# Kernel tuning notes

Hardware: AMD Instinct MI355X
Metric: run time of the kernel (lower is better)

The kernel has to match this reference:

```python
import jax, jax.numpy as jnp
import numpy as np

D_MODEL = 1024
N_HEADS = 16
HEAD_DIM = D_MODEL // N_HEADS
B, T = 4, 2048


def setup_inputs() -> dict:
    key = jax.random.key(0)
    ks = jax.random.split(key, 5)
    x = jax.random.normal(ks[0], (B, T, D_MODEL), dtype=jnp.float32)
    # causal mask; masked_fill(mask == 0, -inf) => attend where mask is True
    mask = jnp.tril(jnp.ones((T, T), dtype=bool))
    # parameters (torch Linear: y = x @ W.T + b); store already-transposed [in, out]
    s_in = 1.0 / np.sqrt(D_MODEL)
    Wqkv = jax.random.uniform(ks[1], (D_MODEL, 3 * D_MODEL), jnp.float32, -s_in, s_in)
    bqkv = jax.random.uniform(ks[2], (3 * D_MODEL,), jnp.float32, -s_in, s_in)
    Wout = jax.random.uniform(ks[3], (D_MODEL, D_MODEL), jnp.float32, -s_in, s_in)
    bout = jax.random.uniform(ks[4], (D_MODEL,), jnp.float32, -s_in, s_in)
    return {"x": x, "mask": mask, "Wqkv": Wqkv, "bqkv": bqkv, "Wout": Wout, "bout": bout}


def reference(x, mask, Wqkv, bqkv, Wout, bout):
    Bq, Tq, C = x.shape
    qkv = x @ Wqkv + bqkv                       # [B, T, 3C]
    q, k, v = jnp.split(qkv, 3, axis=-1)
    def split_heads(t):
        return t.reshape(Bq, Tq, N_HEADS, HEAD_DIM).transpose(0, 2, 1, 3)  # [B,H,T,d]
    q, k, v = split_heads(q), split_heads(k), split_heads(v)
    scale = 1.0 / np.sqrt(HEAD_DIM).astype(np.float32)
    att = jnp.einsum("bhqd,bhkd->bhqk", q, k) * scale  # [B,H,T,T]
    att = jnp.where(mask, att, -jnp.inf)
    att = jax.nn.softmax(att, axis=-1)
    out = jnp.einsum("bhqk,bhkd->bhqd", att, v)         # [B,H,T,d]
    out = out.transpose(0, 2, 1, 3).reshape(Bq, Tq, C)  # [B,T,C]
    return out @ Wout + bout
```

## Files before the change

kernel.cpp:

```cpp
#include <hip/hip_runtime.h>
#include <hip/hip_bf16.h>
#include <cstdint>
#include <cstddef>

#define DMODEL 1024
#define NHEADS 16
#define HDIM 64
#define BATCH 4
#define SEQ 2048
#define MROWS (BATCH*SEQ)
#define N3 (3*DMODEL)
#define BHCNT (BATCH*NHEADS)

typedef __attribute__((ext_vector_type(8))) short short8;
typedef __attribute__((ext_vector_type(4))) short short4v;
typedef __attribute__((ext_vector_type(4))) float f32x4;
typedef __attribute__((ext_vector_type(4))) unsigned int uint4v;

static __device__ __forceinline__ short f2bf(float f) {
  unsigned int u = __builtin_bit_cast(unsigned int, f);
  return (short)((u + 0x7fffu + ((u >> 16) & 1u)) >> 16);
}

static __device__ __forceinline__ unsigned int pack_bf16(float lo, float hi) {
  unsigned int r;
  asm("v_cvt_pk_bf16_f32 %0, %1, %2" : "=v"(r) : "v"(lo), "v"(hi));
  return r;
}

static __device__ __forceinline__ void permlane32_swap(unsigned int& a, unsigned int& b) {
  asm("v_permlane32_swap_b32 %0, %1" : "+v"(a), "+v"(b));
}
static __device__ __forceinline__ void permlane16_swap(unsigned int& a, unsigned int& b) {
  asm("v_permlane16_swap_b32 %0, %1" : "+v"(a), "+v"(b));
}

static __device__ __forceinline__ float fast_exp2(float x) {
#if __has_builtin(__builtin_amdgcn_exp2f)
  return __builtin_amdgcn_exp2f(x);
#else
  return exp2f(x);
#endif
}

static __device__ __forceinline__ void gload16(const void* g, void* l) {
  __builtin_amdgcn_global_load_lds(
      (const __attribute__((address_space(1))) unsigned int*)g,
      (__attribute__((address_space(3))) unsigned int*)l, 16, 0, 0);
}

__global__ __launch_bounds__(256) void cast_x_kernel(
    const float* __restrict__ in, short* __restrict__ out, int n) {
  int i = (blockIdx.x * 256 + threadIdx.x) * 4;
  if (i + 3 < n) {
    float4 v = *(const float4*)(in + i);
    short4v s;
    s[0] = f2bf(v.x); s[1] = f2bf(v.y); s[2] = f2bf(v.z); s[3] = f2bf(v.w);
    *(short4v*)(out + i) = s;
  }
}

__global__ __launch_bounds__(256) void transpose_cast_kernel(
    const float* __restrict__ in, short* __restrict__ out, int K, int N) {
  __shared__ float tile[32][33];
  int n0 = blockIdx.x * 32, k0 = blockIdx.y * 32;
  int tx = threadIdx.x, ty = threadIdx.y;
#pragma unroll
  for (int i = 0; i < 4; ++i)
    tile[ty + i * 8][tx] = in[(size_t)(k0 + ty + i * 8) * N + (n0 + tx)];
  __syncthreads();
#pragma unroll
  for (int i = 0; i < 4; ++i)
    out[(size_t)(n0 + ty + i * 8) * K + (k0 + tx)] = f2bf(tile[tx][ty + i * 8]);
}

template <int EPI>
__global__ __launch_bounds__(256, 2) void gemm128_kernel(
    const short* __restrict__ A, const short* __restrict__ Bt,
    const float* __restrict__ bias, float* __restrict__ foutp,
    short* __restrict__ q_out, short* __restrict__ k_out,
    short* __restrict__ v_out, int Mdim, int Ndim, int Kdim) {
  __shared__ __align__(16) short As[128 * 32];
  __shared__ __align__(16) short Bs[128 * 32];
  const int tid = threadIdx.x;
  const int lane = tid & 63;
  const int w = tid >> 6;
  const int wr = w >> 1, wc = w & 1;
  const int nwg = gridDim.x * gridDim.y;
  const int lin = blockIdx.y * gridDim.x + blockIdx.x;
  const int tile = (lin & 7) * (nwg >> 3) + (lin >> 3);
  const int row0 = (tile / gridDim.x) * 128;
  const int col0 = (tile % gridDim.x) * 128;
  const int lrow = lane & 15, lkg = lane >> 4;

  f32x4 acc[4][4];
#pragma unroll
  for (int i = 0; i < 4; ++i)
#pragma unroll
    for (int j = 0; j < 4; ++j) acc[i][j] = (f32x4){0.f, 0.f, 0.f, 0.f};

  const short* Ab = A + (size_t)row0 * Kdim;
  const short* Bb = Bt + (size_t)col0 * Kdim;
  const int sr = tid >> 2;
  const int sc = (tid & 3) * 8;

  for (int kt = 0; kt < Kdim; kt += 32) {
    gload16(Ab + (size_t)sr * Kdim + kt + sc, As + tid * 8);
    gload16(Ab + (size_t)(sr + 64) * Kdim + kt + sc, As + 2048 + tid * 8);
    gload16(Bb + (size_t)sr * Kdim + kt + sc, Bs + tid * 8);
    gload16(Bb + (size_t)(sr + 64) * Kdim + kt + sc, Bs + 2048 + tid * 8);
    __syncthreads();
    short8 af[4], bfr[4];
#pragma unroll
    for (int i = 0; i < 4; ++i)
      af[i] = *(const short8*)(As + (wr * 64 + i * 16 + lrow) * 32 + lkg * 8);
#pragma unroll
    for (int j = 0; j < 4; ++j)
      bfr[j] = *(const short8*)(Bs + (wc * 64 + j * 16 + lrow) * 32 + lkg * 8);
#pragma unroll
    for (int i = 0; i < 4; ++i)
#pragma unroll
      for (int j = 0; j < 4; ++j)
        acc[i][j] = __builtin_amdgcn_mfma_f32_16x16x32_bf16(af[i], bfr[j], acc[i][j], 0, 0, 0);
    __syncthreads();
  }

#pragma unroll
  for (int i = 0; i < 4; ++i) {
#pragma unroll
    for (int j = 0; j < 4; ++j) {
      const int gn = col0 + wc * 64 + j * 16 + lrow;
      const int gmb = row0 + wr * 64 + i * 16 + lkg * 4;
      float vr[4];
#pragma unroll
      for (int r = 0; r < 4; ++r) vr[r] = acc[i][j][r] + bias[gn];
      if (EPI == 0) {
        const int which = gn >> 10;
        const int hh = (gn >> 6) & 15;
        const int dd = gn & 63;
        const int b = gmb >> 11;
        const int tt0 = gmb & 2047;
        const size_t bh = (size_t)b * NHEADS + hh;
        if (which == 0) {
#pragma unroll
          for (int r = 0; r < 4; ++r)
            q_out[(bh * SEQ + tt0 + r) * HDIM + dd] = f2bf(vr[r] * 0.125f);
        } else if (which == 1) {
#pragma unroll
          for (int r = 0; r < 4; ++r)
            k_out[(bh * SEQ + tt0 + r) * HDIM + (dd ^ (((tt0 + r) & 7) << 3))] = f2bf(vr[r]);
        } else {
          short4v pk;
#pragma unroll
          for (int r = 0; r < 4; ++r) pk[r] = f2bf(vr[r]);
          *(short4v*)(v_out + (bh * HDIM + dd) * SEQ + (tt0 ^ ((dd & 7) << 3))) = pk;
        }
      } else {
#pragma unroll
        for (int r = 0; r < 4; ++r)
          foutp[(size_t)(gmb + r) * Ndim + gn] = vr[r];
      }
    }
  }
}

__global__ __launch_bounds__(256, 4) void attn_kernel(
    const short* __restrict__ qb, const short* __restrict__ kb,
    const short* __restrict__ vb, short* __restrict__ aout) {
  __shared__ __align__(16) short Ks2[2][64 * 64];
  __shared__ __align__(16) short Vs2[2][64 * 64];
  const int tid = threadIdx.x;
  const int lane = tid & 63;
  const int w = tid >> 6;
  const int lin = blockIdx.y * gridDim.x + blockIdx.x;
  const int tile = ((lin & 7) << 7) + (lin >> 3);
  const int bh = tile >> 4;
  const int ip = tile & 15;
  const int heavy_q0 = (31 - ip) * 64;
  const int light_q0 = ip * 64;
  const int qw0 = (w < 2) ? heavy_q0 + w * 32 : light_q0 + (w - 2) * 32;
  const int lrow = lane & 15, lkg = lane >> 4;

  const short* kbase = kb + (size_t)bh * SEQ * HDIM;
  const short* vbase = vb + (size_t)bh * HDIM * SEQ;

  short8 qf[2][2];
#pragma unroll
  for (int rb = 0; rb < 2; ++rb) {
    const short* qrow = qb + ((size_t)bh * SEQ + qw0 + rb * 16 + lrow) * HDIM;
    qf[rb][0] = *(const short8*)(qrow + lkg * 8);
    qf[rb][1] = *(const short8*)(qrow + 32 + lkg * 8);
  }

  f32x4 o[2][4];
  float mr[2], lsum[2];
#pragma unroll
  for (int rb = 0; rb < 2; ++rb) {
#pragma unroll
    for (int g = 0; g < 4; ++g) o[rb][g] = (f32x4){0.f, 0.f, 0.f, 0.f};
    mr[rb] = -__builtin_inff();
    lsum[rb] = 0.f;
  }

  const int ntile = 32 - ip;

  {
    short* Kd = Ks2[0]; short* Vd = Vs2[0];
#pragma unroll
    for (int i = 0; i < 2; ++i)
      gload16(kbase + i * 2048 + tid * 8, Kd + i * 2048 + tid * 8);
#pragma unroll
    for (int i = 0; i < 2; ++i)
      gload16(vbase + (size_t)(32 * i + (tid >> 3)) * SEQ + (tid & 7) * 8,
              Vd + i * 2048 + tid * 8);
  }
  __syncthreads();

  int cur = 0;
  for (int it = 0; it < ntile; ++it) {
    const int kt = it * 64;
    if (it + 1 < ntile) {
      const int k2 = kt + 64;
      short* Kd = Ks2[cur ^ 1]; short* Vd = Vs2[cur ^ 1];
#pragma unroll
      for (int i = 0; i < 2; ++i)
        gload16(kbase + (size_t)k2 * HDIM + i * 2048 + tid * 8, Kd + i * 2048 + tid * 8);
#pragma unroll
      for (int i = 0; i < 2; ++i)
        gload16(vbase + (size_t)(32 * i + (tid >> 3)) * SEQ + k2 + (tid & 7) * 8,
                Vd + i * 2048 + tid * 8);
    }
    if (kt <= qw0 + 31) {
      const short* Ks = Ks2[cur];
      const short* Vs = Vs2[cur];
      f32x4 s[2][4];
#pragma unroll
      for (int rb = 0; rb < 2; ++rb)
#pragma unroll
        for (int f = 0; f < 4; ++f) s[rb][f] = (f32x4){0.f, 0.f, 0.f, 0.f};

      __builtin_amdgcn_s_setprio(1);
#pragma unroll
      for (int c = 0; c < 2; ++c) {
#pragma unroll
        for (int f = 0; f < 4; ++f) {
          const int krow = f * 16 + lrow;
          const int kel = (c * 32 + lkg * 8) ^ ((krow & 7) << 3);
          short8 kf = *(const short8*)(Ks + krow * 64 + kel);
          s[0][f] = __builtin_amdgcn_mfma_f32_16x16x32_bf16(kf, qf[0][c], s[0][f], 0, 0, 0);
          s[1][f] = __builtin_amdgcn_mfma_f32_16x16x32_bf16(kf, qf[1][c], s[1][f], 0, 0, 0);
        }
      }
      __builtin_amdgcn_s_setprio(0);

      if (kt + 63 > qw0) {
#pragma unroll
        for (int rb = 0; rb < 2; ++rb) {
          const int qq = qw0 + rb * 16 + lrow;
#pragma unroll
          for (int f = 0; f < 4; ++f) {
            const int kg = kt + f * 16 + lkg * 4;
#pragma unroll
            for (int r = 0; r < 4; ++r)
              if (kg + r > qq) s[rb][f][r] = -__builtin_inff();
          }
        }
      }

      const float L2E = 1.44269504088896340736f;
      float pm[2];
#pragma unroll
      for (int rb = 0; rb < 2; ++rb) {
        float p = fmaxf(fmaxf(fmaxf(s[rb][0][0], s[rb][0][1]), fmaxf(s[rb][0][2], s[rb][0][3])),
                        fmaxf(fmaxf(s[rb][1][0], s[rb][1][1]), fmaxf(s[rb][1][2], s[rb][1][3])));
        p = fmaxf(p, fmaxf(fmaxf(fmaxf(s[rb][2][0], s[rb][2][1]), fmaxf(s[rb][2][2], s[rb][2][3])),
                           fmaxf(fmaxf(s[rb][3][0], s[rb][3][1]), fmaxf(s[rb][3][2], s[rb][3][3]))));
        p = fmaxf(p, __shfl_xor(p, 16));
        p = fmaxf(p, __shfl_xor(p, 32));
        pm[rb] = p;
      }
      const float mn0 = fmaxf(mr[0], pm[0]);
      const float mn1 = fmaxf(mr[1], pm[1]);
      if (!__all(pm[0] <= mr[0] && pm[1] <= mr[1])) {
        const float a0 = fast_exp2((mr[0] - mn0) * L2E);
        const float a1 = fast_exp2((mr[1] - mn1) * L2E);
        lsum[0] *= a0;
        lsum[1] *= a1;
#pragma unroll
        for (int r = 0; r < 4; ++r) {
          const float s0 = __shfl(a0, lkg * 4 + r, 16);
          const float s1 = __shfl(a1, lkg * 4 + r, 16);
#pragma unroll
          for (int g = 0; g < 4; ++g) { o[0][g][r] *= s0; o[1][g][r] *= s1; }
        }
      }
      mr[0] = mn0; mr[1] = mn1;

      unsigned int q32[2][4][2];
#pragma unroll
      for (int rb = 0; rb < 2; ++rb) {
        const float mn = rb ? mn1 : mn0;
        float rs = 0.f;
#pragma unroll
        for (int f = 0; f < 4; ++f)
#pragma unroll
          for (int r = 0; r < 4; ++r) {
            const float p = fast_exp2((s[rb][f][r] - mn) * L2E);
            s[rb][f][r] = p;
            rs += p;
          }
        rs += __shfl_xor(rs, 16);
        rs += __shfl_xor(rs, 32);
        lsum[rb] += rs;
#pragma unroll
        for (int f = 0; f < 4; ++f) {
          q32[rb][f][0] = pack_bf16(s[rb][f][0], s[rb][f][1]);
          q32[rb][f][1] = pack_bf16(s[rb][f][2], s[rb][f][3]);
        }
      }

      __builtin_amdgcn_s_setprio(1);
#pragma unroll
      for (int c = 0; c < 2; ++c) {
        uint4v pw0, pw1;
#pragma unroll
        for (int h = 0; h < 2; ++h) {
          unsigned int a0 = q32[0][2 * c][h], b0 = q32[0][2 * c + 1][h];
          permlane32_swap(a0, b0);
          permlane16_swap(a0, b0);
          pw0[h] = a0; pw0[2 + h] = b0;
          unsigned int a1 = q32[1][2 * c][h], b1 = q32[1][2 * c + 1][h];
          permlane32_swap(a1, b1);
          permlane16_swap(a1, b1);
          pw1[h] = a1; pw1[2 + h] = b1;
        }
        const short8 pf0 = __builtin_bit_cast(short8, pw0);
        const short8 pf1 = __builtin_bit_cast(short8, pw1);
#pragma unroll
        for (int g = 0; g < 4; ++g) {
          const int vrow = g * 16 + lrow;
          const int vel = (c * 32 + lkg * 8) ^ ((vrow & 7) << 3);
          short8 vf = *(const short8*)(Vs + vrow * 64 + vel);
          o[0][g] = __builtin_amdgcn_mfma_f32_16x16x32_bf16(pf0, vf, o[0][g], 0, 0, 0);
          o[1][g] = __builtin_amdgcn_mfma_f32_16x16x32_bf16(pf1, vf, o[1][g], 0, 0, 0);
        }
      }
      __builtin_amdgcn_s_setprio(0);
    }
    __syncthreads();
    cur ^= 1;
  }

  const int b = bh >> 4, h = bh & 15;
  const float li0 = 1.0f / lsum[0];
  const float li1 = 1.0f / lsum[1];
#pragma unroll
  for (int r = 0; r < 4; ++r) {
    const float i0 = __shfl(li0, lkg * 4 + r, 16);
    const float i1 = __shfl(li1, lkg * 4 + r, 16);
    const int t0 = qw0 + lkg * 4 + r;
#pragma unroll
    for (int g = 0; g < 4; ++g) {
      aout[((size_t)b * SEQ + t0) * DMODEL + h * 64 + g * 16 + lrow] = f2bf(o[0][g][r] * i0);
      aout[((size_t)b * SEQ + t0 + 16) * DMODEL + h * 64 + g * 16 + lrow] = f2bf(o[1][g][r] * i1);
    }
  }
}

extern "C" void kernel_launch(void* const* d_in, const int* in_sizes, int n_in,
                              void* d_out, int out_size, void* d_ws, size_t ws_size,
                              hipStream_t stream) {
  const float* x = (const float*)d_in[0];
  const float* Wqkv = (const float*)d_in[2];
  const float* bqkv = (const float*)d_in[3];
  const float* Wout = (const float*)d_in[4];
  const float* bout = (const float*)d_in[5];

  char* ws = (char*)d_ws;
  short* xb    = (short*)(ws + 0);
  short* wqkvT = (short*)(ws + 16777216);
  short* woutT = (short*)(ws + 23068672);
  short* qbuf  = (short*)(ws + 25165824);
  short* kbuf  = (short*)(ws + 41943040);
  short* vbuf  = (short*)(ws + 58720256);
  short* abuf  = (short*)(ws + 75497472);

  cast_x_kernel<<<(MROWS * DMODEL) / 4 / 256, 256, 0, stream>>>(x, xb, MROWS * DMODEL);
  transpose_cast_kernel<<<dim3(N3 / 32, DMODEL / 32), dim3(32, 8), 0, stream>>>(
      Wqkv, wqkvT, DMODEL, N3);
  transpose_cast_kernel<<<dim3(DMODEL / 32, DMODEL / 32), dim3(32, 8), 0, stream>>>(
      Wout, woutT, DMODEL, DMODEL);
  gemm128_kernel<0><<<dim3(N3 / 128, MROWS / 128), 256, 0, stream>>>(
      xb, wqkvT, bqkv, nullptr, qbuf, kbuf, vbuf, MROWS, N3, DMODEL);
  attn_kernel<<<dim3(16, BHCNT), 256, 0, stream>>>(qbuf, kbuf, vbuf, abuf);
  gemm128_kernel<1><<<dim3(DMODEL / 128, MROWS / 128), 256, 0, stream>>>(
      abuf, woutT, bout, (float*)d_out, nullptr, nullptr, nullptr, MROWS, DMODEL, DMODEL);
}
```

Measured before the change: 287.7 us.

## Balance causal attention work by giving each wave one heavy and one light row block

Previously waves 0-1 handled two 16-row blocks of the heavy query tile and waves 2-3 handled the light tile, so the light waves sat idle for most K tiles. Now every wave owns one 16-row block from the heavy tile and one from the light tile, processing the light block only while it is causally active. This evens out per-wave work inside the block so all four waves stay busy across the K loop. In exchange, the two row blocks no longer share K/V fragment loads from LDS within a single MFMA sequence, so LDS reads per MFMA increase, and softmax bookkeeping is done in two separate passes.

After: 273.8 us. -4.8%, faster.

```diff
diff --git a/kernel.cpp b/kernel.cpp
--- a/kernel.cpp
+++ b/kernel.cpp
@@ -164,6 +164,99 @@
   }
 }
 
+static __device__ __forceinline__ void attn_rb_tile(
+    const short* __restrict__ Ks, const short* __restrict__ Vs,
+    const short8 qf[2], f32x4 o[4], float& mr, float& lsum,
+    bool diag, int kt, int qq, int lrow, int lkg) {
+  f32x4 s[4];
+#pragma unroll
+  for (int f = 0; f < 4; ++f) s[f] = (f32x4){0.f, 0.f, 0.f, 0.f};
+
+  __builtin_amdgcn_s_setprio(1);
+#pragma unroll
+  for (int c = 0; c < 2; ++c) {
+#pragma unroll
+    for (int f = 0; f < 4; ++f) {
+      const int krow = f * 16 + lrow;
+      const int kel = (c * 32 + lkg * 8) ^ ((krow & 7) << 3);
+      short8 kf = *(const short8*)(Ks + krow * 64 + kel);
+      s[f] = __builtin_amdgcn_mfma_f32_16x16x32_bf16(kf, qf[c], s[f], 0, 0, 0);
+    }
+  }
+  __builtin_amdgcn_s_setprio(0);
+
+  if (diag) {
+#pragma unroll
+    for (int f = 0; f < 4; ++f) {
+      const int kg = kt + f * 16 + lkg * 4;
+#pragma unroll
+      for (int r = 0; r < 4; ++r)
+        if (kg + r > qq) s[f][r] = -__builtin_inff();
+    }
+  }
+
+  const float L2E = 1.44269504088896340736f;
+  float pm = fmaxf(fmaxf(fmaxf(s[0][0], s[0][1]), fmaxf(s[0][2], s[0][3])),
+                   fmaxf(fmaxf(s[1][0], s[1][1]), fmaxf(s[1][2], s[1][3])));
+  pm = fmaxf(pm, fmaxf(fmaxf(fmaxf(s[2][0], s[2][1]), fmaxf(s[2][2], s[2][3])),
+                       fmaxf(fmaxf(s[3][0], s[3][1]), fmaxf(s[3][2], s[3][3]))));
+  pm = fmaxf(pm, __shfl_xor(pm, 16));
+  pm = fmaxf(pm, __shfl_xor(pm, 32));
+  const float mn = fmaxf(mr, pm);
+  if (!__all(pm <= mr)) {
+    const float a = fast_exp2((mr - mn) * L2E);
+    lsum *= a;
+#pragma unroll
+    for (int r = 0; r < 4; ++r) {
+      const float ar = __shfl(a, lkg * 4 + r, 16);
+#pragma unroll
+      for (int g = 0; g < 4; ++g) o[g][r] *= ar;
+    }
+  }
+  mr = mn;
+
+  float rf[4];
+#pragma unroll
+  for (int f = 0; f < 4; ++f) {
+#pragma unroll
+    for (int r = 0; r < 4; ++r) s[f][r] = fast_exp2((s[f][r] - mn) * L2E);
+    rf[f] = (s[f][0] + s[f][1]) + (s[f][2] + s[f][3]);
+  }
+  float rs = (rf[0] + rf[1]) + (rf[2] + rf[3]);
+  rs += __shfl_xor(rs, 16);
+  rs += __shfl_xor(rs, 32);
+  lsum += rs;
+
+  unsigned int q32[4][2];
+#pragma unroll
+  for (int f = 0; f < 4; ++f) {
+    q32[f][0] = pack_bf16(s[f][0], s[f][1]);
+    q32[f][1] = pack_bf16(s[f][2], s[f][3]);
+  }
+
+  __builtin_amdgcn_s_setprio(1);
+#pragma unroll
+  for (int c = 0; c < 2; ++c) {
+    uint4v pw;
+#pragma unroll
+    for (int h = 0; h < 2; ++h) {
+      unsigned int a = q32[2 * c][h], b = q32[2 * c + 1][h];
+      permlane32_swap(a, b);
+      permlane16_swap(a, b);
+      pw[h] = a; pw[2 + h] = b;
+    }
+    const short8 pf = __builtin_bit_cast(short8, pw);
+#pragma unroll
+    for (int g = 0; g < 4; ++g) {
+      const int vrow = g * 16 + lrow;
+      const int vel = (c * 32 + lkg * 8) ^ ((vrow & 7) << 3);
+      short8 vf = *(const short8*)(Vs + vrow * 64 + vel);
+      o[g] = __builtin_amdgcn_mfma_f32_16x16x32_bf16(pf, vf, o[g], 0, 0, 0);
+    }
+  }
+  __builtin_amdgcn_s_setprio(0);
+}
+
 __global__ __launch_bounds__(256, 4) void attn_kernel(
     const short* __restrict__ qb, const short* __restrict__ kb,
     const short* __restrict__ vb, short* __restrict__ aout) {
@@ -178,28 +271,30 @@
   const int ip = tile & 15;
   const int heavy_q0 = (31 - ip) * 64;
   const int light_q0 = ip * 64;
-  const int qw0 = (w < 2) ? heavy_q0 + w * 32 : light_q0 + (w - 2) * 32;
+  const int qr0 = heavy_q0 + w * 16;
+  const int qr1 = light_q0 + w * 16;
   const int lrow = lane & 15, lkg = lane >> 4;
 
   const short* kbase = kb + (size_t)bh * SEQ * HDIM;
   const short* vbase = vb + (size_t)bh * HDIM * SEQ;
 
-  short8 qf[2][2];
-#pragma unroll
-  for (int rb = 0; rb < 2; ++rb) {
-    const short* qrow = qb + ((size_t)bh * SEQ + qw0 + rb * 16 + lrow) * HDIM;
-    qf[rb][0] = *(const short8*)(qrow + lkg * 8);
-    qf[rb][1] = *(const short8*)(qrow + 32 + lkg * 8);
-  }
-
-  f32x4 o[2][4];
-  float mr[2], lsum[2];
-#pragma unroll
-  for (int rb = 0; rb < 2; ++rb) {
-#pragma unroll
-    for (int g = 0; g < 4; ++g) o[rb][g] = (f32x4){0.f, 0.f, 0.f, 0.f};
-    mr[rb] = -__builtin_inff();
-    lsum[rb] = 0.f;
+  short8 qf0[2], qf1[2];
+  {
+    const short* qrow = qb + ((size_t)bh * SEQ + qr0 + lrow) * HDIM;
+    qf0[0] = *(const short8*)(qrow + lkg * 8);
+    qf0[1] = *(const short8*)(qrow + 32 + lkg * 8);
+    const short* qrow1 = qb + ((size_t)bh * SEQ + qr1 + lrow) * HDIM;
+    qf1[0] = *(const short8*)(qrow1 + lkg * 8);
+    qf1[1] = *(const short8*)(qrow1 + 32 + lkg * 8);
+  }
+
+  f32x4 o0[4], o1[4];
+  float mr0 = -__builtin_inff(), mr1 = -__builtin_inff();
+  float ls0 = 0.f, ls1 = 0.f;
+#pragma unroll
+  for (int g = 0; g < 4; ++g) {
+    o0[g] = (f32x4){0.f, 0.f, 0.f, 0.f};
+    o1[g] = (f32x4){0.f, 0.f, 0.f, 0.f};
   }
 
   const int ntile = 32 - ip;
@@ -230,139 +325,30 @@
         gload16(vbase + (size_t)(32 * i + (tid >> 3)) * SEQ + k2 + (tid & 7) * 8,
                 Vd + i * 2048 + tid * 8);
     }
-    if (kt <= qw0 + 31) {
-      const short* Ks = Ks2[cur];
-      const short* Vs = Vs2[cur];
-      f32x4 s[2][4];
-#pragma unroll
-      for (int rb = 0; rb < 2; ++rb)
-#pragma unroll
-        for (int f = 0; f < 4; ++f) s[rb][f] = (f32x4){0.f, 0.f, 0.f, 0.f};
-
-      __builtin_amdgcn_s_setprio(1);
-#pragma unroll
-      for (int c = 0; c < 2; ++c) {
-#pragma unroll
-        for (int f = 0; f < 4; ++f) {
-          const int krow = f * 16 + lrow;
-          const int kel = (c * 32 + lkg * 8) ^ ((krow & 7) << 3);
-          short8 kf = *(const short8*)(Ks + krow * 64 + kel);
-          s[0][f] = __builtin_amdgcn_mfma_f32_16x16x32_bf16(kf, qf[0][c], s[0][f], 0, 0, 0);
-          s[1][f] = __builtin_amdgcn_mfma_f32_16x16x32_bf16(kf, qf[1][c], s[1][f], 0, 0, 0);
-        }
-      }
-      __builtin_amdgcn_s_setprio(0);
-
-      if (kt + 63 > qw0) {
-#pragma unroll
-        for (int rb = 0; rb < 2; ++rb) {
-          const int qq = qw0 + rb * 16 + lrow;
-#pragma unroll
-          for (int f = 0; f < 4; ++f) {
-            const int kg = kt + f * 16 + lkg * 4;
-#pragma unroll
-            for (int r = 0; r < 4; ++r)
-              if (kg + r > qq) s[rb][f][r] = -__builtin_inff();
-          }
-        }
-      }
-
-      const float L2E = 1.44269504088896340736f;
-      float pm[2];
-#pragma unroll
-      for (int rb = 0; rb < 2; ++rb) {
-        float p = fmaxf(fmaxf(fmaxf(s[rb][0][0], s[rb][0][1]), fmaxf(s[rb][0][2], s[rb][0][3])),
-                        fmaxf(fmaxf(s[rb][1][0], s[rb][1][1]), fmaxf(s[rb][1][2], s[rb][1][3])));
-        p = fmaxf(p, fmaxf(fmaxf(fmaxf(s[rb][2][0], s[rb][2][1]), fmaxf(s[rb][2][2], s[rb][2][3])),
-                           fmaxf(fmaxf(s[rb][3][0], s[rb][3][1]), fmaxf(s[rb][3][2], s[rb][3][3]))));
-        p = fmaxf(p, __shfl_xor(p, 16));
-        p = fmaxf(p, __shfl_xor(p, 32));
-        pm[rb] = p;
-      }
-      const float mn0 = fmaxf(mr[0], pm[0]);
-      const float mn1 = fmaxf(mr[1], pm[1]);
-      if (!__all(pm[0] <= mr[0] && pm[1] <= mr[1])) {
-        const float a0 = fast_exp2((mr[0] - mn0) * L2E);
-        const float a1 = fast_exp2((mr[1] - mn1) * L2E);
-        lsum[0] *= a0;
-        lsum[1] *= a1;
-#pragma unroll
-        for (int r = 0; r < 4; ++r) {
-          const float s0 = __shfl(a0, lkg * 4 + r, 16);
-          const float s1 = __shfl(a1, lkg * 4 + r, 16);
-#pragma unroll
-          for (int g = 0; g < 4; ++g) { o[0][g][r] *= s0; o[1][g][r] *= s1; }
-        }
-      }
-      mr[0] = mn0; mr[1] = mn1;
-
-      unsigned int q32[2][4][2];
-#pragma unroll
-      for (int rb = 0; rb < 2; ++rb) {
-        const float mn = rb ? mn1 : mn0;
-        float rs = 0.f;
-#pragma unroll
-        for (int f = 0; f < 4; ++f)
-#pragma unroll
-          for (int r = 0; r < 4; ++r) {
-            const float p = fast_exp2((s[rb][f][r] - mn) * L2E);
-            s[rb][f][r] = p;
-            rs += p;
-          }
-        rs += __shfl_xor(rs, 16);
-        rs += __shfl_xor(rs, 32);
-        lsum[rb] += rs;
-#pragma unroll
-        for (int f = 0; f < 4; ++f) {
-          q32[rb][f][0] = pack_bf16(s[rb][f][0], s[rb][f][1]);
-          q32[rb][f][1] = pack_bf16(s[rb][f][2], s[rb][f][3]);
-        }
-      }
-
-      __builtin_amdgcn_s_setprio(1);
-#pragma unroll
-      for (int c = 0; c < 2; ++c) {
-        uint4v pw0, pw1;
-#pragma unroll
-        for (int h = 0; h < 2; ++h) {
-          unsigned int a0 = q32[0][2 * c][h], b0 = q32[0][2 * c + 1][h];
-          permlane32_swap(a0, b0);
-          permlane16_swap(a0, b0);
-          pw0[h] = a0; pw0[2 + h] = b0;
-          unsigned int a1 = q32[1][2 * c][h], b1 = q32[1][2 * c + 1][h];
-          permlane32_swap(a1, b1);
-          permlane16_swap(a1, b1);
-          pw1[h] = a1; pw1[2 + h] = b1;
-        }
-        const short8 pf0 = __builtin_bit_cast(short8, pw0);
-        const short8 pf1 = __builtin_bit_cast(short8, pw1);
-#pragma unroll
-        for (int g = 0; g < 4; ++g) {
-          const int vrow = g * 16 + lrow;
-          const int vel = (c * 32 + lkg * 8) ^ ((vrow & 7) << 3);
-          short8 vf = *(const short8*)(Vs + vrow * 64 + vel);
-          o[0][g] = __builtin_amdgcn_mfma_f32_16x16x32_bf16(pf0, vf, o[0][g], 0, 0, 0);
-          o[1][g] = __builtin_amdgcn_mfma_f32_16x16x32_bf16(pf1, vf, o[1][g], 0, 0, 0);
-        }
-      }
-      __builtin_amdgcn_s_setprio(0);
-    }
+    const short* Ks = Ks2[cur];
+    const short* Vs = Vs2[cur];
+    attn_rb_tile(Ks, Vs, qf0, o0, mr0, ls0,
+                 kt + 63 > qr0, kt, qr0 + lrow, lrow, lkg);
+    if (it <= ip)
+      attn_rb_tile(Ks, Vs, qf1, o1, mr1, ls1,
+                   kt + 63 > qr1, kt, qr1 + lrow, lrow, lkg);
     __syncthreads();
     cur ^= 1;
   }
 
   const int b = bh >> 4, h = bh & 15;
-  const float li0 = 1.0f / lsum[0];
-  const float li1 = 1.0f / lsum[1];
+  const float li0 = 1.0f / ls0;
+  const float li1 = 1.0f / ls1;
 #pragma unroll
   for (int r = 0; r < 4; ++r) {
     const float i0 = __shfl(li0, lkg * 4 + r, 16);
     const float i1 = __shfl(li1, lkg * 4 + r, 16);
-    const int t0 = qw0 + lkg * 4 + r;
+    const int t0 = qr0 + lkg * 4 + r;
+    const int t1 = qr1 + lkg * 4 + r;
 #pragma unroll
     for (int g = 0; g < 4; ++g) {
-      aout[((size_t)b * SEQ + t0) * DMODEL + h * 64 + g * 16 + lrow] = f2bf(o[0][g][r] * i0);
-      aout[((size_t)b * SEQ + t0 + 16) * DMODEL + h * 64 + g * 16 + lrow] = f2bf(o[1][g][r] * i1);
+      aout[((size_t)b * SEQ + t0) * DMODEL + h * 64 + g * 16 + lrow] = f2bf(o0[g][r] * i0);
+      aout[((size_t)b * SEQ + t1) * DMODEL + h * 64 + g * 16 + lrow] = f2bf(o1[g][r] * i1);
     }
   }
 }
```
